# Kernel optimization log

Hardware: AMD Instinct MI355X
Metric: run time of the kernel (lower is better)

## Reference

```python
import jax, jax.numpy as jnp
import numpy as np

NUM_CLASSES = 1000
FEATURE_DIM = 256
TEMPERATURE = 0.07
EPS = 1e-12  # matches torch F.normalize default eps


def setup_inputs() -> dict:
    key = jax.random.key(0)
    k1, k2, k3, k4 = jax.random.split(key, 4)
    N = 200000
    return {
        "src_feats": jax.random.normal(k1, (N, FEATURE_DIM), dtype=jnp.float32),
        "src_labels": jax.random.randint(k2, (N,), 0, NUM_CLASSES, dtype=jnp.int64),
        "tgt_feats": jax.random.normal(k3, (N, FEATURE_DIM), dtype=jnp.float32),
        "tgt_labels": jax.random.randint(k4, (N,), 0, NUM_CLASSES, dtype=jnp.int64),
    }


def _l2_normalize(x):
    norm = jnp.sqrt(jnp.sum(x * x, axis=1, keepdims=True))
    return x / jnp.maximum(norm, EPS)


def _prototype_init(features, labels):
    """Single-pass segment-mean replacing the per-class python loop.
    prototypes[c] = mean of features with label==c (0 if class absent)."""
    sums = jax.ops.segment_sum(features, labels, num_segments=NUM_CLASSES)  # [C, D]
    counts = jax.ops.segment_sum(jnp.ones_like(labels, dtype=features.dtype),
                                 labels, num_segments=NUM_CLASSES)          # [C]
    protos = sums / jnp.maximum(counts, 1.0)[:, None]
    return protos, counts


def _structure_matrix(protos):
    p = _l2_normalize(protos)
    return p @ p.T  # [C, C]


def reference(src_feats, src_labels, tgt_feats, tgt_labels):
    # PrototypeBank.update with detached features (first call: plain segment-mean)
    src_protos, _ = _prototype_init(jax.lax.stop_gradient(src_feats), src_labels)
    tgt_protos, _ = _prototype_init(jax.lax.stop_gradient(tgt_feats), tgt_labels)

    src_struct = _structure_matrix(src_protos)
    tgt_struct = _structure_matrix(tgt_protos)
    struct_loss = jnp.mean((src_struct - tgt_struct) ** 2)

    # contrastive loss: cosine logits against source prototypes, cross-entropy
    feats_n = _l2_normalize(src_feats)
    protos_n = _l2_normalize(src_protos)
    logits = (feats_n @ protos_n.T) / TEMPERATURE  # [N, C]
    logp = jax.nn.log_softmax(logits, axis=1)
    contrast_loss = -jnp.mean(jnp.take_along_axis(logp, src_labels[:, None], axis=1))

    return struct_loss, contrast_loss, src_protos, src_struct
```

## Files before the change

kernel.cpp:

```cpp
#include <hip/hip_runtime.h>
#include <hip/hip_fp8.h>

#define NCLS 1000
#define DIM 256
#define GCAP 500
#define NT16 64
#define SCLF 20.609930f
#define CP 23.0f
#define CPLN2 15.94238515f
#define LN2 0.69314718056f
#define PADC 2.86102294921875e-06f

typedef __attribute__((ext_vector_type(4))) float f32x4;
typedef long long i64;
typedef unsigned long long u64;

#if defined(__has_builtin) && __has_builtin(__builtin_amdgcn_cvt_pk_fp8_f32)
#define CVTPK(a, b, old, hi) __builtin_amdgcn_cvt_pk_fp8_f32((a), (b), (old), (hi))
#else
__device__ __forceinline__ unsigned cvtpk_sw(float a, float b, unsigned old, bool hi) {
  unsigned lo8 = __hip_cvt_float_to_fp8(a, __HIP_SATFINITE, __HIP_E4M3);
  unsigned hi8 = __hip_cvt_float_to_fp8(b, __HIP_SATFINITE, __HIP_E4M3);
  unsigned pk = lo8 | (hi8 << 8);
  return hi ? ((old & 0xffffu) | (pk << 16)) : ((old & 0xffff0000u) | pk);
}
#define CVTPK(a, b, old, hi) cvtpk_sw((a), (b), (old), (hi))
#endif

__device__ __forceinline__ float fexp2(float x) {
#if __has_builtin(__builtin_amdgcn_exp2f)
  return __builtin_amdgcn_exp2f(x);
#else
  return exp2f(x);
#endif
}

__global__ __launch_bounds__(256) void scatter_kernel(
    const int* __restrict__ sl, const int* __restrict__ tl, int N,
    int* __restrict__ gcnt, int* __restrict__ glist) {
  const int i = blockIdx.x * 256 + threadIdx.x;
  if (i >= 2 * N) return;
  const int side = (i >= N) ? 1 : 0;
  const int r = i - side * N;
  const int c = (side ? tl : sl)[r];
  const int bin = side * NCLS + c;
  const int slot = atomicAdd(gcnt + bin, 1);
  if (slot < GCAP) glist[(size_t)bin * GCAP + slot] = r;
}

__global__ __launch_bounds__(256) void proto_kernel(
    const float* __restrict__ sf, const float* __restrict__ tf,
    const int* __restrict__ gcnt, const int* __restrict__ glist,
    float* __restrict__ mean_out, float* __restrict__ spn, float* __restrict__ tpn,
    unsigned char* __restrict__ pbf8) {
  const int bid = blockIdx.x;
  const int side = (bid < NCLS) ? 1 : 0;
  const int c = side ? bid : (bid - NCLS);
  const int bin = side * NCLS + c;
  const float* feats = side ? tf : sf;
  const int* list = glist + (size_t)bin * GCAP;
  const int m = min(gcnt[bin], GCAP);
  const int t = threadIdx.x;
  __shared__ float s_red[4];

  float a0 = 0.f, a1 = 0.f, a2 = 0.f, a3 = 0.f, a4 = 0.f, a5 = 0.f, a6 = 0.f, a7 = 0.f;
  int i = 0;
  for (; i + 8 <= m; i += 8) {
    a0 += feats[(size_t)list[i + 0] * DIM + t];
    a1 += feats[(size_t)list[i + 1] * DIM + t];
    a2 += feats[(size_t)list[i + 2] * DIM + t];
    a3 += feats[(size_t)list[i + 3] * DIM + t];
    a4 += feats[(size_t)list[i + 4] * DIM + t];
    a5 += feats[(size_t)list[i + 5] * DIM + t];
    a6 += feats[(size_t)list[i + 6] * DIM + t];
    a7 += feats[(size_t)list[i + 7] * DIM + t];
  }
  for (; i < m; i++) a0 += feats[(size_t)list[i] * DIM + t];
  const float sum = ((a0 + a1) + (a2 + a3)) + ((a4 + a5) + (a6 + a7));
  const float mean = sum / fmaxf((float)m, 1.0f);
  if (!side) mean_out[(size_t)c * DIM + t] = mean;

  float ss = mean * mean;
  #pragma unroll
  for (int o = 1; o < 64; o <<= 1) ss += __shfl_xor(ss, o);
  if ((t & 63) == 0) s_red[t >> 6] = ss;
  __syncthreads();
  const float tot = s_red[0] + s_red[1] + s_red[2] + s_red[3];
  const float innv = 1.0f / fmaxf(sqrtf(tot), 1e-12f);
  const float p = mean * innv;
  (side ? tpn : spn)[(size_t)c * DIM + t] = p;
  if (!side) {
    size_t off = (size_t)(c >> 4) * 4096 + (size_t)(t >> 6) * 1024
               + (size_t)((t >> 3) & 3) * 256 + (size_t)(c & 15) * 16
               + (size_t)((t >> 5) & 1) * 8 + (t & 7);
    unsigned q = CVTPK(p, p, 0u, false);
    pbf8[off] = (unsigned char)(q & 0xffu);
  }
}

__global__ __launch_bounds__(256, 2) void fused_kernel(
    const float* __restrict__ feats, const int* __restrict__ labels,
    const unsigned char* __restrict__ pbf8, float* __restrict__ accp,
    const float* __restrict__ spn, const float* __restrict__ tpn,
    float* __restrict__ out_struct, float* __restrict__ acc,
    int N, int cblocks) {
  const int bid = blockIdx.x;
  const int t = threadIdx.x;

  if (bid >= cblocks) {
    const int sbid = bid - cblocks;
    __shared__ float Sa[16][68], Sb[16][68], Ta[16][68], Tb[16][68];
    __shared__ float red[256];
    const int tx = t & 15, ty = t >> 4;
    const int i0 = (sbid >> 4) * 64, j0 = (sbid & 15) * 64;
    float cs[4][4], cg[4][4];
    #pragma unroll
    for (int a = 0; a < 4; a++)
      #pragma unroll
      for (int b = 0; b < 4; b++) { cs[a][b] = 0.f; cg[a][b] = 0.f; }

    const int srow = t >> 2;
    const int skq = (t & 3) * 4;
    for (int k0 = 0; k0 < DIM; k0 += 16) {
      __syncthreads();
      {
        float4 z = make_float4(0.f, 0.f, 0.f, 0.f);
        int ra = i0 + srow, rb = j0 + srow;
        float4 va = (ra < NCLS) ? *(const float4*)(spn + (size_t)ra * DIM + k0 + skq) : z;
        float4 vb = (rb < NCLS) ? *(const float4*)(spn + (size_t)rb * DIM + k0 + skq) : z;
        float4 wa = (ra < NCLS) ? *(const float4*)(tpn + (size_t)ra * DIM + k0 + skq) : z;
        float4 wb = (rb < NCLS) ? *(const float4*)(tpn + (size_t)rb * DIM + k0 + skq) : z;
        Sa[skq+0][srow]=va.x; Sa[skq+1][srow]=va.y; Sa[skq+2][srow]=va.z; Sa[skq+3][srow]=va.w;
        Sb[skq+0][srow]=vb.x; Sb[skq+1][srow]=vb.y; Sb[skq+2][srow]=vb.z; Sb[skq+3][srow]=vb.w;
        Ta[skq+0][srow]=wa.x; Ta[skq+1][srow]=wa.y; Ta[skq+2][srow]=wa.z; Ta[skq+3][srow]=wa.w;
        Tb[skq+0][srow]=wb.x; Tb[skq+1][srow]=wb.y; Tb[skq+2][srow]=wb.z; Tb[skq+3][srow]=wb.w;
      }
      __syncthreads();
      #pragma unroll
      for (int k = 0; k < 16; k++) {
        float a[4], b[4], c[4], d[4];
        *(float4*)a = *(const float4*)&Sa[k][ty * 4];
        *(float4*)b = *(const float4*)&Sb[k][tx * 4];
        *(float4*)c = *(const float4*)&Ta[k][ty * 4];
        *(float4*)d = *(const float4*)&Tb[k][tx * 4];
        #pragma unroll
        for (int ii = 0; ii < 4; ii++)
          #pragma unroll
          for (int jj = 0; jj < 4; jj++) {
            cs[ii][jj] = fmaf(a[ii], b[jj], cs[ii][jj]);
            cg[ii][jj] = fmaf(c[ii], d[jj], cg[ii][jj]);
          }
      }
    }
    float d2 = 0.f;
    #pragma unroll
    for (int ii = 0; ii < 4; ii++) {
      int gi = i0 + ty * 4 + ii;
      if (gi < NCLS) {
        #pragma unroll
        for (int jj = 0; jj < 4; jj++) {
          int gj = j0 + tx * 4 + jj;
          if (gj < NCLS) {
            out_struct[(size_t)gi * NCLS + gj] = cs[ii][jj];
            float df = cs[ii][jj] - cg[ii][jj];
            d2 += df * df;
          }
        }
      }
    }
    red[t] = d2;
    __syncthreads();
    for (int o = 128; o > 0; o >>= 1) { if (t < o) red[t] += red[t + o]; __syncthreads(); }
    if (t == 0) atomicAdd(acc, red[0]);
    return;
  }

  const int lane = t & 63;
  const int lx = lane & 15, lg = lane >> 4;
  const int row0 = bid * 128 + (t >> 6) * 32;
  const float4 z4 = make_float4(0.f, 0.f, 0.f, 0.f);

  i64 af[2][8];
  float sclF[2][4];
  float sSt[2][4], labD[2][4];
  int codeP[2];

  #pragma unroll
  for (int rf = 0; rf < 2; rf++) {
    const int r = row0 + rf * 16 + lx;
    const bool v = r < N;
    const float* rp = feats + (size_t)r * DIM + (lg << 3);
    float n2 = 0.f;
    #pragma unroll
    for (int kf = 0; kf < 8; kf++) {
      float4 x = v ? *(const float4*)(rp + kf * 32)     : z4;
      float4 y = v ? *(const float4*)(rp + kf * 32 + 4) : z4;
      n2 += x.x*x.x + x.y*x.y + x.z*x.z + x.w*x.w
          + y.x*y.x + y.y*y.y + y.z*y.z + y.w*y.w;
      unsigned w0 = CVTPK(x.x, x.y, 0u, false);
      w0 = CVTPK(x.z, x.w, w0, true);
      unsigned w1 = CVTPK(y.x, y.y, 0u, false);
      w1 = CVTPK(y.z, y.w, w1, true);
      af[rf][kf] = (i64)(((u64)w1 << 32) | (u64)w0);
    }
    n2 += __shfl_xor(n2, 16);
    n2 += __shfl_xor(n2, 32);
    const float sw = SCLF / fmaxf(sqrtf(n2), 1e-12f);
    int pc = 0;
    #pragma unroll
    for (int reg = 0; reg < 4; reg++) {
      sclF[rf][reg] = __shfl(sw, (lg << 2) | reg);
      const int row = row0 + rf * 16 + (lg << 2) + reg;
      const int lb = (row < N) ? labels[row] : -1;
      const int tc = (lb >= 0 && (lb & 15) == lx) ? (lb >> 4) : 255;
      pc |= tc << (reg * 8);
      sSt[rf][reg] = 0.f;
      labD[rf][reg] = 0.f;
    }
    codeP[rf] = pc;
  }

  const unsigned char* bbase = pbf8 + (lg << 8) + (lx << 4);
  int4 b0[4], b1[4], b2[4];

  #define LOADB(dst_, cf_)                                                      \
    {                                                                           \
      const int4* gp = (const int4*)(bbase + ((size_t)(cf_) << 12));            \
      _Pragma("unroll")                                                         \
      for (int q = 0; q < 4; q++) dst_[q] = gp[q << 6];                         \
    }

  #define COMPUTE(buf_, g_)                                                     \
    {                                                                           \
      f32x4 d0 = {0.f, 0.f, 0.f, 0.f};                                          \
      f32x4 d1 = {0.f, 0.f, 0.f, 0.f};                                          \
      _Pragma("unroll")                                                         \
      for (int q = 0; q < 4; q++) {                                             \
        i64 e0 = ((const i64*)&buf_[q])[0];                                     \
        i64 e1 = ((const i64*)&buf_[q])[1];                                     \
        d0 = __builtin_amdgcn_mfma_f32_16x16x32_fp8_fp8(af[0][2*q],   e0, d0, 0, 0, 0); \
        d1 = __builtin_amdgcn_mfma_f32_16x16x32_fp8_fp8(af[1][2*q],   e0, d1, 0, 0, 0); \
        d0 = __builtin_amdgcn_mfma_f32_16x16x32_fp8_fp8(af[0][2*q+1], e1, d0, 0, 0, 0); \
        d1 = __builtin_amdgcn_mfma_f32_16x16x32_fp8_fp8(af[1][2*q+1], e1, d1, 0, 0, 0); \
      }                                                                         \
      _Pragma("unroll")                                                         \
      for (int reg = 0; reg < 4; reg++) {                                       \
        sSt[0][reg] += fexp2(fmaf(d0[reg], sclF[0][reg], -CP));                 \
        sSt[1][reg] += fexp2(fmaf(d1[reg], sclF[1][reg], -CP));                 \
        labD[0][reg] += (((codeP[0] >> (reg * 8)) & 255) == (g_)) ? d0[reg] : 0.f; \
        labD[1][reg] += (((codeP[1] >> (reg * 8)) & 255) == (g_)) ? d1[reg] : 0.f; \
      }                                                                         \
    }

  LOADB(b0, 0);
  LOADB(b1, 1);
  int cf = 0;
  for (; cf + 3 <= NT16; cf += 3) {
    LOADB(b2, cf + 2);
    COMPUTE(b0, cf);
    if (cf + 3 < NT16) LOADB(b0, cf + 3);
    COMPUTE(b1, cf + 1);
    if (cf + 4 < NT16) LOADB(b1, cf + 4);
    COMPUTE(b2, cf + 2);
  }
  if (cf < NT16) COMPUTE(b0, cf);

  float wl = 0.f;
  #pragma unroll
  for (int rf = 0; rf < 2; rf++)
    #pragma unroll
    for (int reg = 0; reg < 4; reg++) {
      float s = sSt[rf][reg], lb = labD[rf][reg];
      #pragma unroll
      for (int o = 1; o < 16; o <<= 1) { s += __shfl_xor(s, o); lb += __shfl_xor(lb, o); }
      const int row = row0 + rf * 16 + (lg << 2) + reg;
      if (lx == 0 && row < N)
        wl += logf(s - PADC) + CPLN2 - lb * sclF[rf][reg] * LN2;
    }

  #pragma unroll
  for (int o = 1; o < 64; o <<= 1) wl += __shfl_xor(wl, o);
  if (lane == 0) atomicAdd(accp + (bid & 63), wl);
}

__global__ void final_kernel(const float* __restrict__ acc,
                             const float* __restrict__ accp,
                             float* __restrict__ out, int N) {
  float c = 0.f;
  for (int i = 0; i < 64; i++) c += accp[i];
  out[0] = acc[0] * (1.0f / (float)(NCLS * NCLS));
  out[1] = c / (float)N;
}

extern "C" void kernel_launch(void* const* d_in, const int* in_sizes, int n_in,
                              void* d_out, int out_size, void* d_ws, size_t ws_size,
                              hipStream_t stream) {
  const float* src_feats  = (const float*)d_in[0];
  const int*   src_labels = (const int*)d_in[1];
  const float* tgt_feats  = (const float*)d_in[2];
  const int*   tgt_labels = (const int*)d_in[3];
  const int N = in_sizes[0] / DIM;

  float* ws = (float*)d_ws;
  float* acc    = ws;
  float* src_pn = ws + 16;
  float* tgt_pn = ws + 256016;
  unsigned char* pbf8 = (unsigned char*)(ws + 512016);
  int* gcnt = (int*)(ws + 643088);
  float* accp = ws + 645088;

  float* out_f      = (float*)d_out;
  float* out_protos = out_f + 2;
  float* out_struct = out_f + 2 + NCLS * DIM;
  int* glist = (int*)out_struct;

  hipMemsetAsync(acc, 0, 2 * sizeof(float), stream);
  hipMemsetAsync(gcnt, 0, 2 * NCLS * sizeof(int), stream);
  hipMemsetAsync(accp, 0, 64 * sizeof(float), stream);
  hipMemsetAsync(pbf8 + 62 * 4096, 0, 2 * 4096, stream);

  int sblocks = (2 * N + 255) / 256;
  scatter_kernel<<<sblocks, 256, 0, stream>>>(src_labels, tgt_labels, N, gcnt, glist);

  proto_kernel<<<2 * NCLS, 256, 0, stream>>>(src_feats, tgt_feats, gcnt, glist,
                                             out_protos, src_pn, tgt_pn, pbf8);

  int cblocks = (N + 127) / 128;
  fused_kernel<<<cblocks + 256, 256, 0, stream>>>(
      src_feats, src_labels, pbf8, accp, src_pn, tgt_pn, out_struct, acc, N, cblocks);

  final_kernel<<<1, 1, 0, stream>>>(acc, accp, out_f, N);
}
```

Before: 361.8 us.

## Compute label logit via fp32 dot, split MFMA chains, two chunks per block

Drops the per-tile label-match accumulation from the MFMA inner loop and instead computes each row's label logit as an exact fp32 dot product against the normalized source prototype after the loop. Each tile's MFMA work is split into four independent accumulators to shorten dependency chains. The software pipeline goes from triple to double buffering to cut register use. Struct blocks move to the front of the grid and each contrastive block now handles two row chunks, halving the grid. The costs are a second read of the feature rows plus a gather of prototype rows, and less parallelism per launch.

```diff
diff --git a/kernel.cpp b/kernel.cpp
--- a/kernel.cpp
+++ b/kernel.cpp
@@ -103,12 +103,12 @@
     const unsigned char* __restrict__ pbf8, float* __restrict__ accp,
     const float* __restrict__ spn, const float* __restrict__ tpn,
     float* __restrict__ out_struct, float* __restrict__ acc,
-    int N, int cblocks) {
+    int N, int cblocks, int cgrid) {
   const int bid = blockIdx.x;
   const int t = threadIdx.x;
 
-  if (bid >= cblocks) {
-    const int sbid = bid - cblocks;
+  if (bid < 256) {
+    const int sbid = bid;
     __shared__ float Sa[16][68], Sb[16][68], Ta[16][68], Tb[16][68];
     __shared__ float red[256];
     const int tx = t & 15, ty = t >> 4;
@@ -175,112 +175,138 @@
     return;
   }
 
+  const int cbid = bid - 256;
   const int lane = t & 63;
   const int lx = lane & 15, lg = lane >> 4;
-  const int row0 = bid * 128 + (t >> 6) * 32;
   const float4 z4 = make_float4(0.f, 0.f, 0.f, 0.f);
-
-  i64 af[2][8];
-  float sclF[2][4];
-  float sSt[2][4], labD[2][4];
-  int codeP[2];
-
-  #pragma unroll
-  for (int rf = 0; rf < 2; rf++) {
-    const int r = row0 + rf * 16 + lx;
-    const bool v = r < N;
-    const float* rp = feats + (size_t)r * DIM + (lg << 3);
-    float n2 = 0.f;
-    #pragma unroll
-    for (int kf = 0; kf < 8; kf++) {
-      float4 x = v ? *(const float4*)(rp + kf * 32)     : z4;
-      float4 y = v ? *(const float4*)(rp + kf * 32 + 4) : z4;
-      n2 += x.x*x.x + x.y*x.y + x.z*x.z + x.w*x.w
-          + y.x*y.x + y.y*y.y + y.z*y.z + y.w*y.w;
-      unsigned w0 = CVTPK(x.x, x.y, 0u, false);
-      w0 = CVTPK(x.z, x.w, w0, true);
-      unsigned w1 = CVTPK(y.x, y.y, 0u, false);
-      w1 = CVTPK(y.z, y.w, w1, true);
-      af[rf][kf] = (i64)(((u64)w1 << 32) | (u64)w0);
-    }
-    n2 += __shfl_xor(n2, 16);
-    n2 += __shfl_xor(n2, 32);
-    const float sw = SCLF / fmaxf(sqrtf(n2), 1e-12f);
-    int pc = 0;
-    #pragma unroll
-    for (int reg = 0; reg < 4; reg++) {
-      sclF[rf][reg] = __shfl(sw, (lg << 2) | reg);
-      const int row = row0 + rf * 16 + (lg << 2) + reg;
-      const int lb = (row < N) ? labels[row] : -1;
-      const int tc = (lb >= 0 && (lb & 15) == lx) ? (lb >> 4) : 255;
-      pc |= tc << (reg * 8);
-      sSt[rf][reg] = 0.f;
-      labD[rf][reg] = 0.f;
-    }
-    codeP[rf] = pc;
+  const unsigned char* bbase = pbf8 + (lg << 8) + (lx << 4);
+
+  for (int ch = 0; ch < 2; ch++) {
+    const int cchunk = cbid + ch * cgrid;
+    if (cchunk >= cblocks) break;
+    const int row0 = cchunk * 128 + (t >> 6) * 32;
+
+    i64 af[2][8];
+    float sclF[2][4];
+    float sSt[2][4];
+
+    #pragma unroll
+    for (int rf = 0; rf < 2; rf++) {
+      const int r = row0 + rf * 16 + lx;
+      const bool v = r < N;
+      const float* rp = feats + (size_t)r * DIM + (lg << 3);
+      float n2 = 0.f;
+      #pragma unroll
+      for (int kf = 0; kf < 8; kf++) {
+        float4 x = v ? *(const float4*)(rp + kf * 32)     : z4;
+        float4 y = v ? *(const float4*)(rp + kf * 32 + 4) : z4;
+        n2 += x.x*x.x + x.y*x.y + x.z*x.z + x.w*x.w
+            + y.x*y.x + y.y*y.y + y.z*y.z + y.w*y.w;
+        unsigned w0 = CVTPK(x.x, x.y, 0u, false);
+        w0 = CVTPK(x.z, x.w, w0, true);
+        unsigned w1 = CVTPK(y.x, y.y, 0u, false);
+        w1 = CVTPK(y.z, y.w, w1, true);
+        af[rf][kf] = (i64)(((u64)w1 << 32) | (u64)w0);
+      }
+      n2 += __shfl_xor(n2, 16);
+      n2 += __shfl_xor(n2, 32);
+      const float sw = SCLF / fmaxf(sqrtf(n2), 1e-12f);
+      #pragma unroll
+      for (int reg = 0; reg < 4; reg++) {
+        sclF[rf][reg] = __shfl(sw, (lg << 2) | reg);
+        sSt[rf][reg] = 0.f;
+      }
+    }
+
+    int4 bA[4], bB[4];
+
+    #define LOADB(dst_, cf_)                                                    \
+      {                                                                         \
+        const int4* gp = (const int4*)(bbase + ((size_t)(cf_) << 12));          \
+        _Pragma("unroll")                                                       \
+        for (int q = 0; q < 4; q++) dst_[q] = gp[q << 6];                       \
+      }
+
+    #define COMPUTE(buf_)                                                       \
+      {                                                                         \
+        f32x4 dA = {0.f,0.f,0.f,0.f}, dB = {0.f,0.f,0.f,0.f};                   \
+        f32x4 dC = {0.f,0.f,0.f,0.f}, dD = {0.f,0.f,0.f,0.f};                   \
+        _Pragma("unroll")                                                       \
+        for (int q = 0; q < 2; q++) {                                           \
+          i64 e0 = ((const i64*)&buf_[q])[0];                                   \
+          i64 e1 = ((const i64*)&buf_[q])[1];                                   \
+          dA = __builtin_amdgcn_mfma_f32_16x16x32_fp8_fp8(af[0][2*q],   e0, dA, 0, 0, 0); \
+          dC = __builtin_amdgcn_mfma_f32_16x16x32_fp8_fp8(af[1][2*q],   e0, dC, 0, 0, 0); \
+          dA = __builtin_amdgcn_mfma_f32_16x16x32_fp8_fp8(af[0][2*q+1], e1, dA, 0, 0, 0); \
+          dC = __builtin_amdgcn_mfma_f32_16x16x32_fp8_fp8(af[1][2*q+1], e1, dC, 0, 0, 0); \
+        }                                                                       \
+        _Pragma("unroll")                                                       \
+        for (int q = 2; q < 4; q++) {                                           \
+          i64 e0 = ((const i64*)&buf_[q])[0];                                   \
+          i64 e1 = ((const i64*)&buf_[q])[1];                                   \
+          dB = __builtin_amdgcn_mfma_f32_16x16x32_fp8_fp8(af[0][2*q],   e0, dB, 0, 0, 0); \
+          dD = __builtin_amdgcn_mfma_f32_16x16x32_fp8_fp8(af[1][2*q],   e0, dD, 0, 0, 0); \
+          dB = __builtin_amdgcn_mfma_f32_16x16x32_fp8_fp8(af[0][2*q+1], e1, dB, 0, 0, 0); \
+          dD = __builtin_amdgcn_mfma_f32_16x16x32_fp8_fp8(af[1][2*q+1], e1, dD, 0, 0, 0); \
+        }                                                                       \
+        _Pragma("unroll")                                                       \
+        for (int reg = 0; reg < 4; reg++) {                                     \
+          sSt[0][reg] += fexp2(fmaf(dA[reg] + dB[reg], sclF[0][reg], -CP));     \
+          sSt[1][reg] += fexp2(fmaf(dC[reg] + dD[reg], sclF[1][reg], -CP));     \
+        }                                                                       \
+      }
+
+    LOADB(bA, 0);
+    for (int cf = 0; cf < NT16; cf += 2) {
+      LOADB(bB, cf + 1);
+      COMPUTE(bA);
+      if (cf + 2 < NT16) LOADB(bA, cf + 2);
+      COMPUTE(bB);
+    }
+
+    __builtin_amdgcn_sched_barrier(0);
+
+    float dotS[2];
+    #pragma unroll
+    for (int rf = 0; rf < 2; rf++) {
+      const int r = row0 + rf * 16 + lx;
+      const bool v = r < N;
+      const float* rp = feats + (size_t)r * DIM + (lg << 3);
+      const int lb = v ? labels[r] : 0;
+      const float* pp = spn + (size_t)lb * DIM + (lg << 3);
+      float pl = 0.f;
+      #pragma unroll
+      for (int kf = 0; kf < 8; kf++) {
+        float4 x  = v ? *(const float4*)(rp + kf * 32)     : z4;
+        float4 px = v ? *(const float4*)(pp + kf * 32)     : z4;
+        float4 y  = v ? *(const float4*)(rp + kf * 32 + 4) : z4;
+        float4 py = v ? *(const float4*)(pp + kf * 32 + 4) : z4;
+        pl += x.x*px.x + x.y*px.y + x.z*px.z + x.w*px.w
+            + y.x*py.x + y.y*py.y + y.z*py.z + y.w*py.w;
+      }
+      pl += __shfl_xor(pl, 16);
+      pl += __shfl_xor(pl, 32);
+      dotS[rf] = pl;
+    }
+
+    float wl = 0.f;
+    #pragma unroll
+    for (int rf = 0; rf < 2; rf++)
+      #pragma unroll
+      for (int reg = 0; reg < 4; reg++) {
+        float s = sSt[rf][reg];
+        #pragma unroll
+        for (int o = 1; o < 16; o <<= 1) s += __shfl_xor(s, o);
+        const float lbdot = __shfl(dotS[rf], (lg << 2) + reg);
+        const int row = row0 + rf * 16 + (lg << 2) + reg;
+        if (lx == 0 && row < N)
+          wl += logf(s - PADC) + CPLN2 - lbdot * sclF[rf][reg] * LN2;
+      }
+
+    #pragma unroll
+    for (int o = 1; o < 64; o <<= 1) wl += __shfl_xor(wl, o);
+    if (lane == 0) atomicAdd(accp + (cchunk & 63), wl);
   }
-
-  const unsigned char* bbase = pbf8 + (lg << 8) + (lx << 4);
-  int4 b0[4], b1[4], b2[4];
-
-  #define LOADB(dst_, cf_)                                                      \
-    {                                                                           \
-      const int4* gp = (const int4*)(bbase + ((size_t)(cf_) << 12));            \
-      _Pragma("unroll")                                                         \
-      for (int q = 0; q < 4; q++) dst_[q] = gp[q << 6];                         \
-    }
-
-  #define COMPUTE(buf_, g_)                                                     \
-    {                                                                           \
-      f32x4 d0 = {0.f, 0.f, 0.f, 0.f};                                          \
-      f32x4 d1 = {0.f, 0.f, 0.f, 0.f};                                          \
-      _Pragma("unroll")                                                         \
-      for (int q = 0; q < 4; q++) {                                             \
-        i64 e0 = ((const i64*)&buf_[q])[0];                                     \
-        i64 e1 = ((const i64*)&buf_[q])[1];                                     \
-        d0 = __builtin_amdgcn_mfma_f32_16x16x32_fp8_fp8(af[0][2*q],   e0, d0, 0, 0, 0); \
-        d1 = __builtin_amdgcn_mfma_f32_16x16x32_fp8_fp8(af[1][2*q],   e0, d1, 0, 0, 0); \
-        d0 = __builtin_amdgcn_mfma_f32_16x16x32_fp8_fp8(af[0][2*q+1], e1, d0, 0, 0, 0); \
-        d1 = __builtin_amdgcn_mfma_f32_16x16x32_fp8_fp8(af[1][2*q+1], e1, d1, 0, 0, 0); \
-      }                                                                         \
-      _Pragma("unroll")                                                         \
-      for (int reg = 0; reg < 4; reg++) {                                       \
-        sSt[0][reg] += fexp2(fmaf(d0[reg], sclF[0][reg], -CP));                 \
-        sSt[1][reg] += fexp2(fmaf(d1[reg], sclF[1][reg], -CP));                 \
-        labD[0][reg] += (((codeP[0] >> (reg * 8)) & 255) == (g_)) ? d0[reg] : 0.f; \
-        labD[1][reg] += (((codeP[1] >> (reg * 8)) & 255) == (g_)) ? d1[reg] : 0.f; \
-      }                                                                         \
-    }
-
-  LOADB(b0, 0);
-  LOADB(b1, 1);
-  int cf = 0;
-  for (; cf + 3 <= NT16; cf += 3) {
-    LOADB(b2, cf + 2);
-    COMPUTE(b0, cf);
-    if (cf + 3 < NT16) LOADB(b0, cf + 3);
-    COMPUTE(b1, cf + 1);
-    if (cf + 4 < NT16) LOADB(b1, cf + 4);
-    COMPUTE(b2, cf + 2);
-  }
-  if (cf < NT16) COMPUTE(b0, cf);
-
-  float wl = 0.f;
-  #pragma unroll
-  for (int rf = 0; rf < 2; rf++)
-    #pragma unroll
-    for (int reg = 0; reg < 4; reg++) {
-      float s = sSt[rf][reg], lb = labD[rf][reg];
-      #pragma unroll
-      for (int o = 1; o < 16; o <<= 1) { s += __shfl_xor(s, o); lb += __shfl_xor(lb, o); }
-      const int row = row0 + rf * 16 + (lg << 2) + reg;
-      if (lx == 0 && row < N)
-        wl += logf(s - PADC) + CPLN2 - lb * sclF[rf][reg] * LN2;
-    }
-
-  #pragma unroll
-  for (int o = 1; o < 64; o <<= 1) wl += __shfl_xor(wl, o);
-  if (lane == 0) atomicAdd(accp + (bid & 63), wl);
 }
 
 __global__ void final_kernel(const float* __restrict__ acc,
@@ -326,8 +352,10 @@
                                              out_protos, src_pn, tgt_pn, pbf8);
 
   int cblocks = (N + 127) / 128;
-  fused_kernel<<<cblocks + 256, 256, 0, stream>>>(
-      src_feats, src_labels, pbf8, accp, src_pn, tgt_pn, out_struct, acc, N, cblocks);
+  int cgrid = (cblocks + 1) / 2;
+  fused_kernel<<<256 + cgrid, 256, 0, stream>>>(
+      src_feats, src_labels, pbf8, accp, src_pn, tgt_pn, out_struct, acc,
+      N, cblocks, cgrid);
 
   final_kernel<<<1, 1, 0, stream>>>(acc, accp, out_f, N);
 }
```

Result: slower. 623.9 us (+72.5%).

## Compute label logit with a separate MFMA gather and raise occupancy

Applied to the files above, without the earlier changes.

Removes the per-tile label-match select and accumulation from the inner class loop. Instead, each row's true-class logit is computed once after the loop by gathering that class's prototype tile and running a small extra set of MFMAs. The change also moves the structure-matrix blocks to the front of the grid so they start first, switches from triple to double buffering of the B tiles, and raises launch bounds to 3 blocks per CU. Together these cut VALU work and register pressure in the hot loop. The cost is the extra MFMA gather per row and less prefetch depth to hide load latency.

```diff
diff --git a/kernel.cpp b/kernel.cpp
--- a/kernel.cpp
+++ b/kernel.cpp
@@ -98,7 +98,7 @@
   }
 }
 
-__global__ __launch_bounds__(256, 2) void fused_kernel(
+__global__ __launch_bounds__(256, 3) void fused_kernel(
     const float* __restrict__ feats, const int* __restrict__ labels,
     const unsigned char* __restrict__ pbf8, float* __restrict__ accp,
     const float* __restrict__ spn, const float* __restrict__ tpn,
@@ -107,12 +107,11 @@
   const int bid = blockIdx.x;
   const int t = threadIdx.x;
 
-  if (bid >= cblocks) {
-    const int sbid = bid - cblocks;
+  if (bid < 256) {
     __shared__ float Sa[16][68], Sb[16][68], Ta[16][68], Tb[16][68];
     __shared__ float red[256];
     const int tx = t & 15, ty = t >> 4;
-    const int i0 = (sbid >> 4) * 64, j0 = (sbid & 15) * 64;
+    const int i0 = (bid >> 4) * 64, j0 = (bid & 15) * 64;
     float cs[4][4], cg[4][4];
     #pragma unroll
     for (int a = 0; a < 4; a++)
@@ -175,21 +174,25 @@
     return;
   }
 
+  const int cbid = bid - 256;
+  if (cbid >= cblocks) return;
   const int lane = t & 63;
   const int lx = lane & 15, lg = lane >> 4;
-  const int row0 = bid * 128 + (t >> 6) * 32;
+  const int row0 = cbid * 128 + (t >> 6) * 32;
   const float4 z4 = make_float4(0.f, 0.f, 0.f, 0.f);
+  const unsigned char* bbase = pbf8 + (lg << 8) + (lx << 4);
 
   i64 af[2][8];
   float sclF[2][4];
-  float sSt[2][4], labD[2][4];
-  int codeP[2];
+  float sSt[2][4];
+  int lbR[2];
 
   #pragma unroll
   for (int rf = 0; rf < 2; rf++) {
     const int r = row0 + rf * 16 + lx;
     const bool v = r < N;
     const float* rp = feats + (size_t)r * DIM + (lg << 3);
+    lbR[rf] = v ? labels[r] : 0;
     float n2 = 0.f;
     #pragma unroll
     for (int kf = 0; kf < 8; kf++) {
@@ -206,22 +209,14 @@
     n2 += __shfl_xor(n2, 16);
     n2 += __shfl_xor(n2, 32);
     const float sw = SCLF / fmaxf(sqrtf(n2), 1e-12f);
-    int pc = 0;
     #pragma unroll
     for (int reg = 0; reg < 4; reg++) {
       sclF[rf][reg] = __shfl(sw, (lg << 2) | reg);
-      const int row = row0 + rf * 16 + (lg << 2) + reg;
-      const int lb = (row < N) ? labels[row] : -1;
-      const int tc = (lb >= 0 && (lb & 15) == lx) ? (lb >> 4) : 255;
-      pc |= tc << (reg * 8);
       sSt[rf][reg] = 0.f;
-      labD[rf][reg] = 0.f;
-    }
-    codeP[rf] = pc;
-  }
-
-  const unsigned char* bbase = pbf8 + (lg << 8) + (lx << 4);
-  int4 b0[4], b1[4], b2[4];
+    }
+  }
+
+  int4 bA[4], bB[4];
 
   #define LOADB(dst_, cf_)                                                      \
     {                                                                           \
@@ -230,7 +225,7 @@
       for (int q = 0; q < 4; q++) dst_[q] = gp[q << 6];                         \
     }
 
-  #define COMPUTE(buf_, g_)                                                     \
+  #define COMPUTE(buf_)                                                         \
     {                                                                           \
       f32x4 d0 = {0.f, 0.f, 0.f, 0.f};                                          \
       f32x4 d1 = {0.f, 0.f, 0.f, 0.f};                                          \
@@ -247,40 +242,54 @@
       for (int reg = 0; reg < 4; reg++) {                                       \
         sSt[0][reg] += fexp2(fmaf(d0[reg], sclF[0][reg], -CP));                 \
         sSt[1][reg] += fexp2(fmaf(d1[reg], sclF[1][reg], -CP));                 \
-        labD[0][reg] += (((codeP[0] >> (reg * 8)) & 255) == (g_)) ? d0[reg] : 0.f; \
-        labD[1][reg] += (((codeP[1] >> (reg * 8)) & 255) == (g_)) ? d1[reg] : 0.f; \
       }                                                                         \
     }
 
-  LOADB(b0, 0);
-  LOADB(b1, 1);
-  int cf = 0;
-  for (; cf + 3 <= NT16; cf += 3) {
-    LOADB(b2, cf + 2);
-    COMPUTE(b0, cf);
-    if (cf + 3 < NT16) LOADB(b0, cf + 3);
-    COMPUTE(b1, cf + 1);
-    if (cf + 4 < NT16) LOADB(b1, cf + 4);
-    COMPUTE(b2, cf + 2);
-  }
-  if (cf < NT16) COMPUTE(b0, cf);
+  LOADB(bA, 0);
+  for (int cf = 0; cf < NT16; cf += 2) {
+    LOADB(bB, cf + 1);
+    COMPUTE(bA);
+    if (cf + 2 < NT16) LOADB(bA, cf + 2);
+    COMPUTE(bB);
+  }
+
+  float dvalS[2];
+  #pragma unroll
+  for (int rf = 0; rf < 2; rf++) {
+    const int lb = lbR[rf];
+    const unsigned char* gB = pbf8 + ((size_t)(lb >> 4) << 12) + (lg << 8)
+                            + ((size_t)(lb & 15) << 4);
+    f32x4 dL = {0.f, 0.f, 0.f, 0.f};
+    #pragma unroll
+    for (int q = 0; q < 4; q++) {
+      int4 bg = *(const int4*)(gB + (q << 10));
+      i64 e0 = ((const i64*)&bg)[0];
+      i64 e1 = ((const i64*)&bg)[1];
+      dL = __builtin_amdgcn_mfma_f32_16x16x32_fp8_fp8(af[rf][2*q],   e0, dL, 0, 0, 0);
+      dL = __builtin_amdgcn_mfma_f32_16x16x32_fp8_fp8(af[rf][2*q+1], e1, dL, 0, 0, 0);
+    }
+    const int sel = lx & 3;
+    dvalS[rf] = (sel == 0) ? dL[0] : (sel == 1) ? dL[1] : (sel == 2) ? dL[2] : dL[3];
+  }
 
   float wl = 0.f;
   #pragma unroll
   for (int rf = 0; rf < 2; rf++)
     #pragma unroll
     for (int reg = 0; reg < 4; reg++) {
-      float s = sSt[rf][reg], lb = labD[rf][reg];
+      float s = sSt[rf][reg];
       #pragma unroll
-      for (int o = 1; o < 16; o <<= 1) { s += __shfl_xor(s, o); lb += __shfl_xor(lb, o); }
-      const int row = row0 + rf * 16 + (lg << 2) + reg;
+      for (int o = 1; o < 16; o <<= 1) s += __shfl_xor(s, o);
+      const int j = (lg << 2) + reg;
+      const float lbraw = __shfl(dvalS[rf], ((j >> 2) << 4) | j);
+      const int row = row0 + rf * 16 + j;
       if (lx == 0 && row < N)
-        wl += logf(s - PADC) + CPLN2 - lb * sclF[rf][reg] * LN2;
+        wl += logf(s - PADC) + CPLN2 - lbraw * sclF[rf][reg] * LN2;
     }
 
   #pragma unroll
   for (int o = 1; o < 64; o <<= 1) wl += __shfl_xor(wl, o);
-  if (lane == 0) atomicAdd(accp + (bid & 63), wl);
+  if (lane == 0) atomicAdd(accp + (cbid & 63), wl);
 }
 
 __global__ void final_kernel(const float* __restrict__ acc,
@@ -326,7 +335,7 @@
                                              out_protos, src_pn, tgt_pn, pbf8);
 
   int cblocks = (N + 127) / 128;
-  fused_kernel<<<cblocks + 256, 256, 0, stream>>>(
+  fused_kernel<<<256 + cblocks, 256, 0, stream>>>(
       src_feats, src_labels, pbf8, accp, src_pn, tgt_pn, out_struct, acc, N, cblocks);
 
   final_kernel<<<1, 1, 0, stream>>>(acc, accp, out_f, N);
```

Measured after the change: 368.8 us. No clear change (+1.9%).
